# Performance work log

Measured on AMD Instinct MI355X. Metric: run time of the kernel, lower is better.

## Reference

```python
import jax, jax.numpy as jnp
import numpy as np

B, S, D, H = 2, 2048, 1024, 16
DK = D // H  # 64

def setup_inputs() -> dict:
    key = jax.random.key(0)
    ks = jax.random.split(key, 12)
    scale = 1.0 / np.sqrt(D)
    return {
        "q": jax.random.normal(ks[0], (B, S, D), jnp.float32),
        "k": jax.random.normal(ks[1], (B, S, D), jnp.float32),
        "v": jax.random.normal(ks[2], (B, S, D), jnp.float32),
        "Wq": jax.random.normal(ks[3], (D, D), jnp.float32) * scale,
        "bq": jnp.zeros((D,), jnp.float32),
        "Wk": jax.random.normal(ks[4], (D, D), jnp.float32) * scale,
        "bk": jnp.zeros((D,), jnp.float32),
        "Wv": jax.random.normal(ks[5], (D, D), jnp.float32) * scale,
        "bv": jnp.zeros((D,), jnp.float32),
        "Wo": jax.random.normal(ks[6], (D, D), jnp.float32) * scale,
        "bo": jnp.zeros((D,), jnp.float32),
        "mask": jnp.ones((B, 1, S, S), jnp.bool_),
    }

def reference(q, k, v, Wq, bq, Wk, bk, Wv, bv, Wo, bo, mask):
    # Linear projections: y = x @ W^T + b (torch nn.Linear convention)
    def proj(x, W, b):
        return x @ W.T + b
    # [B,S,D] -> [B,H,S,DK]
    def split_heads(x):
        return x.reshape(B, S, H, DK).transpose(0, 2, 1, 3)

    query = split_heads(proj(q, Wq, bq))
    key_ = split_heads(proj(k, Wk, bk))
    value = split_heads(proj(v, Wv, bv))

    # NOTE: original uses out-of-place masked_fill whose result is discarded,
    # so mask has no effect on the computation (reproduced faithfully here).
    scores = jnp.einsum('bhqd,bhkd->bhqk', query, key_) / jnp.sqrt(
        jnp.asarray(DK, query.dtype))
    attn = jax.nn.softmax(scores, axis=-1)  # dropout p=0.0: identity
    x = jnp.einsum('bhqk,bhkd->bhqd', attn, value)
    x = x.transpose(0, 2, 1, 3).reshape(B, S, D)
    return proj(x, Wo, bo)
```

## Files before the change

### kernel.cpp

```cpp
#include <hip/hip_runtime.h>
#include <hip/hip_bf16.h>


typedef __attribute__((ext_vector_type(8))) short bf16x8;
typedef __attribute__((ext_vector_type(4))) float f32x4;
typedef unsigned short u16;
typedef unsigned int u32;

#define MFMA16(a, b, c) __builtin_amdgcn_mfma_f32_16x16x32_bf16(a, b, c, 0, 0, 0)
#define EXP2(x) __builtin_amdgcn_exp2f(x)

static __device__ __forceinline__ u16 f2bf(float f) {
    union { __hip_bfloat16 h; u16 u; } v;
    v.h = __float2bfloat16(f);
    return v.u;
}

static __device__ __forceinline__ u16 f2bf_fast(float f) {
    return (u16)((__float_as_uint(f) + 0x8000u) >> 16);
}

static __device__ __forceinline__ void gload16(const u16* g, u16* l) {
    __builtin_amdgcn_global_load_lds(
        (const __attribute__((address_space(1))) void*)g,
        (__attribute__((address_space(3))) void*)l, 16, 0, 0);
}

struct CvtArgs { const float* in[4]; u16* out[4]; };

__global__ __launch_bounds__(256)
void cvt_multi(CvtArgs a, int bp)
{
    const int tsel = blockIdx.x / bp;
    const int i = ((blockIdx.x % bp) * 256 + threadIdx.x) * 8;
    const float* in = a.in[tsel];
    u16* out = a.out[tsel];
    float4 x = *(const float4*)(in + i);
    float4 y = *(const float4*)(in + i + 4);
    u16 o[8];
    o[0]=f2bf(x.x); o[1]=f2bf(x.y); o[2]=f2bf(x.z); o[3]=f2bf(x.w);
    o[4]=f2bf(y.x); o[5]=f2bf(y.y); o[6]=f2bf(y.z); o[7]=f2bf(y.w);
    *(uint4*)(out + i) = *(uint4*)o;
}

struct GemmArgs {
    const u16* A[3]; const u16* W[3]; const float* bias[3];
    u16* C[3]; float osc[3]; int epi[3];
};

__global__ __launch_bounds__(256)
void gemm_qkv(GemmArgs g)
{
    __shared__ u16 lds_a[2][128 * 32];
    __shared__ u16 lds_b[2][128 * 32];

    const int z = blockIdx.y;
    const u16* Ap = g.A[z];
    const u16* Wp = g.W[z];
    const int epi = g.epi[z];

    const int t    = threadIdx.x;
    const int lane = t & 63;
    const int w    = t >> 6;
    const int wm   = w >> 1, wn = w & 1;
    const int ll   = lane & 15;
    const int lg   = lane >> 4;

    const int tile_m = (epi == 1 ? (blockIdx.x & 7) : (blockIdx.x >> 3)) * 128;
    const int tile_n = (epi == 1 ? (blockIdx.x >> 3) : (blockIdx.x & 7)) * 128;

    const int c0   = w * 2;
    const int lrow = lane >> 2;
    const int lcol = (lane & 3) * 8;

    f32x4 acc[4][4] = {};

    #define STAGE(buf, kt)                                                     \
    {                                                                          \
        _Pragma("unroll")                                                      \
        for (int j = 0; j < 2; j++) {                                          \
            const int c = c0 + j;                                              \
            gload16(Ap + (size_t)(tile_m + c * 16 + lrow) * 1024 + (kt) + lcol,\
                    &lds_a[buf][c * 512]);                                     \
            gload16(Wp + (size_t)(tile_n + c * 16 + lrow) * 1024 + (kt) + lcol,\
                    &lds_b[buf][c * 512]);                                     \
        }                                                                      \
    }

    STAGE(0, 0);
    __syncthreads();

    int cur = 0;
    for (int kt = 0; kt < 1024; kt += 32) {
        if (kt + 32 < 1024) STAGE(cur ^ 1, kt + 32);

        bf16x8 af[4], bfr[4];
        #pragma unroll
        for (int i = 0; i < 4; i++)
            af[i] = *(bf16x8*)&lds_a[cur][(wm * 64 + i * 16 + ll) * 32 + lg * 8];
        #pragma unroll
        for (int j = 0; j < 4; j++)
            bfr[j] = *(bf16x8*)&lds_b[cur][(wn * 64 + j * 16 + ll) * 32 + lg * 8];
        #pragma unroll
        for (int i = 0; i < 4; i++)
            #pragma unroll
            for (int j = 0; j < 4; j++)
                acc[i][j] = MFMA16(af[i], bfr[j], acc[i][j]);

        __syncthreads();
        cur ^= 1;
    }
    #undef STAGE

    const float osc = g.osc[z];
    const float* bias = g.bias[z];
    u16* Cp = g.C[z];

    #pragma unroll
    for (int i = 0; i < 4; i++) {
        const int row0 = tile_m + wm * 64 + i * 16 + lg * 4;
        #pragma unroll
        for (int j = 0; j < 4; j++) {
            const int col = tile_n + wn * 64 + j * 16 + ll;
            if (epi == 1) {
                const int b = col >> 11, s = col & 2047;
                #pragma unroll
                for (int r = 0; r < 4; r++)
                    Cp[(size_t)(b * 1024 + row0 + r) * 2048 + s] =
                        f2bf(acc[i][j][r] + bias[row0 + r]);
            } else {
                const float bias_v = bias[col];
                const int h = col >> 6, dk = col & 63;
                const int b = row0 >> 11;
                #pragma unroll
                for (int r = 0; r < 4; r++) {
                    const int s = (row0 + r) & 2047;
                    Cp[((size_t)(b * 16 + h) * 2048 + s) * 64 + dk] =
                        f2bf((acc[i][j][r] + bias_v) * osc);
                }
            }
        }
    }
}

__global__ __launch_bounds__(256)
void gemm_out(const u16* __restrict__ Ap, const u16* __restrict__ Wp,
              const float* __restrict__ bias, float* __restrict__ Cp)
{
    __shared__ u16 lds_a[2][128 * 32];
    __shared__ u16 lds_b[2][64 * 32];

    const int t    = threadIdx.x;
    const int lane = t & 63;
    const int w    = t >> 6;
    const int wm   = w >> 1, wn = w & 1;
    const int ll   = lane & 15;
    const int lg   = lane >> 4;

    const int tile_m = (blockIdx.x >> 4) * 128;
    const int tile_n = (blockIdx.x & 15) * 64;

    const int lrow = lane >> 2;
    const int lcol = (lane & 3) * 8;

    f32x4 acc[4][2] = {};

    #define OSTAGE(buf, kt)                                                    \
    {                                                                          \
        _Pragma("unroll")                                                      \
        for (int j = 0; j < 3; j++) {                                          \
            const int c = w * 3 + j;                                           \
            if (c < 8) {                                                       \
                const int row = tile_m + c * 16 + lrow;                        \
                const int col = (kt) + lcol;                                   \
                const u16* ga = Ap + ((size_t)((row >> 11) * 16 + (col >> 6))  \
                                      * 2048 + (row & 2047)) * 64 + (col & 63);\
                gload16(ga, &lds_a[buf][c * 512]);                             \
            } else {                                                           \
                const int cc = c - 8;                                          \
                gload16(Wp + (size_t)(tile_n + cc * 16 + lrow) * 1024          \
                        + (kt) + lcol, &lds_b[buf][cc * 512]);                 \
            }                                                                  \
        }                                                                      \
    }

    OSTAGE(0, 0);
    __syncthreads();

    int cur = 0;
    for (int kt = 0; kt < 1024; kt += 32) {
        if (kt + 32 < 1024) OSTAGE(cur ^ 1, kt + 32);

        bf16x8 af[4], bfr[2];
        #pragma unroll
        for (int i = 0; i < 4; i++)
            af[i] = *(bf16x8*)&lds_a[cur][(wm * 64 + i * 16 + ll) * 32 + lg * 8];
        #pragma unroll
        for (int j = 0; j < 2; j++)
            bfr[j] = *(bf16x8*)&lds_b[cur][(wn * 32 + j * 16 + ll) * 32 + lg * 8];
        #pragma unroll
        for (int i = 0; i < 4; i++)
            #pragma unroll
            for (int j = 0; j < 2; j++)
                acc[i][j] = MFMA16(af[i], bfr[j], acc[i][j]);

        __syncthreads();
        cur ^= 1;
    }
    #undef OSTAGE

    #pragma unroll
    for (int i = 0; i < 4; i++) {
        const int row0 = tile_m + wm * 64 + i * 16 + lg * 4;
        #pragma unroll
        for (int j = 0; j < 2; j++) {
            const int col = tile_n + wn * 32 + j * 16 + ll;
            const float bias_v = bias[col];
            #pragma unroll
            for (int r = 0; r < 4; r++)
                Cp[(size_t)(row0 + r) * 1024 + col] = acc[i][j][r] + bias_v;
        }
    }
}

__global__ __launch_bounds__(512)
void attn_kernel(const u16* __restrict__ Qh, const u16* __restrict__ Kh,
                 const u16* __restrict__ Vt, u16* __restrict__ Oh)
{
    __shared__ u16 lds_k[2][64 * 64];
    __shared__ u16 lds_v[2][64 * 64];
    __shared__ u16 lds_p[8][16 * 64];

    const int t    = threadIdx.x;
    const int lane = t & 63;
    const int w    = t >> 6;
    const int ll   = lane & 15;
    const int lg   = lane >> 4;
    const int r7   = ll & 7;

    const int qt = blockIdx.x & 15;
    const int bh = blockIdx.x >> 4;
    const int q0 = qt * 128 + w * 16;

    const u16* Qbase = Qh + ((size_t)bh * 2048 + q0 + ll) * 64 + lg * 8;
    const bf16x8 bq0 = *(const bf16x8*)(Qbase);
    const bf16x8 bq1 = *(const bf16x8*)(Qbase + 32);

    bf16x8 bones;
    #pragma unroll
    for (int i = 0; i < 8; i++) bones[i] = (short)0x3F80;

    f32x4 acc[4] = {};
    f32x4 acc_l = {};
    float m_run = 0.f;

    const int srow = lane >> 3;
    const int scol = 8 * ((lane & 7) ^ srow);
    const u16* Kg = Kh + (size_t)bh * 2048 * 64;
    const u16* Vg = Vt + (size_t)bh * 64 * 2048;

    #define ASTAGE(buf, kt)                                                    \
    {                                                                          \
        const int rr = w * 8 + srow;                                           \
        gload16(Kg + (size_t)((kt) + rr) * 64 + scol, &lds_k[buf][w * 512]);   \
        gload16(Vg + (size_t)rr * 2048 + (kt) + scol, &lds_v[buf][w * 512]);   \
    }

    ASTAGE(0, 0);
    __syncthreads();

    u16* lp = lds_p[w];
    int cur = 0;

    for (int kt = 0; kt < 2048; kt += 64) {
        if (kt + 64 < 2048) ASTAGE(cur ^ 1, kt + 64);

        f32x4 s[4];
        #pragma unroll
        for (int ks = 0; ks < 4; ks++) {
            const u16* kp = &lds_k[cur][(ks * 16 + ll) * 64];
            const bf16x8 ak0 = *(const bf16x8*)(kp + ((lg * 8)      ^ (r7 * 8)));
            const bf16x8 ak1 = *(const bf16x8*)(kp + ((lg * 8 + 32) ^ (r7 * 8)));
            f32x4 z = {-m_run, -m_run, -m_run, -m_run};
            z = MFMA16(ak0, bq0, z);
            z = MFMA16(ak1, bq1, z);
            s[ks] = z;
        }

        float m0 = fmaxf(fmaxf(s[0][0], s[0][1]), s[0][2]);
        float m1 = fmaxf(fmaxf(s[0][3], s[1][0]), s[1][1]);
        float m2 = fmaxf(fmaxf(s[1][2], s[1][3]), s[2][0]);
        float m3 = fmaxf(fmaxf(s[2][1], s[2][2]), s[2][3]);
        float m4 = fmaxf(fmaxf(s[3][0], s[3][1]), s[3][2]);
        float mx = fmaxf(fmaxf(fmaxf(m0, m1), fmaxf(m2, m3)),
                         fmaxf(m4, s[3][3]));
        mx = fmaxf(mx, __shfl_xor(mx, 16));
        mx = fmaxf(mx, __shfl_xor(mx, 32));

        if (!__all(mx <= 11.0f)) {
            const float dsh = fmaxf(mx, 0.f);
            const float es = EXP2(-dsh);
            m_run += dsh;
            #pragma unroll
            for (int r = 0; r < 4; r++) {
                const float esq = __shfl(es, lg * 4 + r);
                #pragma unroll
                for (int dt = 0; dt < 4; dt++) acc[dt][r] *= esq;
                acc_l[r] *= esq;
            }
            #pragma unroll
            for (int ks = 0; ks < 4; ks++) {
                u16 pk[4];
                #pragma unroll
                for (int r = 0; r < 4; r++) pk[r] = f2bf_fast(EXP2(s[ks][r] - dsh));
                *(uint2*)&lp[ll * 64 + ((ks * 16 + lg * 4) ^ (r7 * 8))] = *(uint2*)pk;
            }
        } else {
            #pragma unroll
            for (int ks = 0; ks < 4; ks++) {
                u16 pk[4];
                #pragma unroll
                for (int r = 0; r < 4; r++) pk[r] = f2bf_fast(EXP2(s[ks][r]));
                *(uint2*)&lp[ll * 64 + ((ks * 16 + lg * 4) ^ (r7 * 8))] = *(uint2*)pk;
            }
        }

        #pragma unroll
        for (int ks2 = 0; ks2 < 2; ks2++) {
            const int so = (ks2 * 32 + lg * 8) ^ (r7 * 8);
            const bf16x8 pa = *(const bf16x8*)&lp[ll * 64 + so];
            #pragma unroll
            for (int dt = 0; dt < 4; dt++) {
                const bf16x8 bv = *(const bf16x8*)&lds_v[cur][(dt * 16 + ll) * 64 + so];
                acc[dt] = MFMA16(pa, bv, acc[dt]);
            }
            acc_l = MFMA16(pa, bones, acc_l);
        }

        __syncthreads();
        cur ^= 1;
    }
    #undef ASTAGE

    #pragma unroll
    for (int r = 0; r < 4; r++) {
        const float lq = 1.f / acc_l[r];
        const int qg = q0 + lg * 4 + r;
        u16* Op = Oh + ((size_t)bh * 2048 + qg) * 64 + ll;
        #pragma unroll
        for (int dt = 0; dt < 4; dt++)
            Op[dt * 16] = f2bf(acc[dt][r] * lq);
    }
}

extern "C" void kernel_launch(void* const* d_in, const int* in_sizes, int n_in,
                              void* d_out, int out_size, void* d_ws, size_t ws_size,
                              hipStream_t stream) {
    const float* q  = (const float*)d_in[0];
    const float* k  = (const float*)d_in[1];
    const float* v  = (const float*)d_in[2];
    const float* Wq = (const float*)d_in[3];
    const float* bq = (const float*)d_in[4];
    const float* Wk = (const float*)d_in[5];
    const float* bk = (const float*)d_in[6];
    const float* Wv = (const float*)d_in[7];
    const float* bv = (const float*)d_in[8];
    const float* Wo = (const float*)d_in[9];
    const float* bo = (const float*)d_in[10];
    float* out = (float*)d_out;

    const size_t M4 = (size_t)4 * 1024 * 1024;
    const size_t M1 = (size_t)1024 * 1024;
    const float qscale = 0.18033688011112042f;
    const dim3 blk(256);

    if (ws_size >= (size_t)56 * 1024 * 1024) {
        u16* Xq  = (u16*)d_ws;
        u16* Xk  = Xq + M4;
        u16* Xv  = Xk + M4;
        u16* Qh  = Xv + M4;
        u16* Kh  = Qh + M4;
        u16* Vtb = Kh + M4;
        u16* Wqb = Vtb + M4;
        u16* Wkb = Wqb + M1;
        u16* Wvb = Wkb + M1;
        u16* Wob = Wvb + M1;
        u16* Oh  = Xq;

        CvtArgs cw; cw.in[0]=Wq; cw.in[1]=Wk; cw.in[2]=Wv; cw.in[3]=Wo;
        cw.out[0]=Wqb; cw.out[1]=Wkb; cw.out[2]=Wvb; cw.out[3]=Wob;
        cvt_multi<<<4 * 512, blk, 0, stream>>>(cw, 512);

        CvtArgs cx; cx.in[0]=q; cx.in[1]=k; cx.in[2]=v; cx.in[3]=q;
        cx.out[0]=Xq; cx.out[1]=Xk; cx.out[2]=Xv; cx.out[3]=Xq;
        cvt_multi<<<3 * 2048, blk, 0, stream>>>(cx, 2048);

        GemmArgs ga;
        ga.A[0]=Xq;  ga.A[1]=Xk;  ga.A[2]=Wvb;
        ga.W[0]=Wqb; ga.W[1]=Wkb; ga.W[2]=Xv;
        ga.bias[0]=bq; ga.bias[1]=bk; ga.bias[2]=bv;
        ga.C[0]=Qh; ga.C[1]=Kh; ga.C[2]=Vtb;
        ga.osc[0]=qscale; ga.osc[1]=1.0f; ga.osc[2]=1.0f;
        ga.epi[0]=3; ga.epi[1]=3; ga.epi[2]=1;
        gemm_qkv<<<dim3(256, 3), blk, 0, stream>>>(ga);

        attn_kernel<<<512, dim3(512), 0, stream>>>(Qh, Kh, Vtb, Oh);

        gemm_out<<<512, blk, 0, stream>>>(Oh, Wob, bo, out);
    } else {
        u16* X   = (u16*)d_ws;
        u16* Qh  = X + M4;
        u16* Kh  = Qh + M4;
        u16* Vtb = Kh + M4;
        u16* Wqb = Vtb + M4;
        u16* Wkb = Wqb + M1;
        u16* Wvb = Wkb + M1;
        u16* Wob = Wvb + M1;

        CvtArgs cw; cw.in[0]=Wq; cw.in[1]=Wk; cw.in[2]=Wv; cw.in[3]=Wo;
        cw.out[0]=Wqb; cw.out[1]=Wkb; cw.out[2]=Wvb; cw.out[3]=Wob;
        cvt_multi<<<4 * 512, blk, 0, stream>>>(cw, 512);

        const float* srcs[3] = {q, k, v};
        for (int i = 0; i < 3; i++) {
            CvtArgs cx; cx.in[0]=srcs[i]; cx.out[0]=X;
            cx.in[1]=cx.in[2]=cx.in[3]=srcs[i]; cx.out[1]=cx.out[2]=cx.out[3]=X;
            cvt_multi<<<2048, blk, 0, stream>>>(cx, 2048);
            GemmArgs ga;
            for (int z = 0; z < 3; z++) {
                if (i == 2) { ga.A[z]=Wvb; ga.W[z]=X;  ga.C[z]=Vtb; ga.bias[z]=bv; ga.osc[z]=1.0f; ga.epi[z]=1; }
                else if (i == 0) { ga.A[z]=X; ga.W[z]=Wqb; ga.C[z]=Qh; ga.bias[z]=bq; ga.osc[z]=qscale; ga.epi[z]=3; }
                else { ga.A[z]=X; ga.W[z]=Wkb; ga.C[z]=Kh; ga.bias[z]=bk; ga.osc[z]=1.0f; ga.epi[z]=3; }
            }
            gemm_qkv<<<dim3(256, 1), blk, 0, stream>>>(ga);
        }

        attn_kernel<<<512, dim3(512), 0, stream>>>(Qh, Kh, Vtb, X);

        gemm_out<<<512, blk, 0, stream>>>(X, Wob, bo, out);
    }
}
```

Before: 145.5 us.

## Merge conversions into one launch, swizzle block IDs, and prioritize MFMA phases

Merges the weight and activation fp32-to-bf16 conversions into a single launch of 16 equal-size slices, saving one kernel launch. Remaps block indices in both GEMMs and the attention kernel with an XCD-aware swizzle, so that consecutive blocks sharing the same data land on the same chiplet's L2. In attention it raises wave priority around the MFMA sections with s_setprio. It also skips the cross-lane max reduction unless the rescale branch is actually taken. The per-lane __all check stays equivalent because the row max is only needed when rescaling.

```diff
diff --git a/kernel.cpp b/kernel.cpp
--- a/kernel.cpp
+++ b/kernel.cpp
@@ -26,13 +26,13 @@
         (__attribute__((address_space(3))) void*)l, 16, 0, 0);
 }
 
-struct CvtArgs { const float* in[4]; u16* out[4]; };
+struct CvtArgs16 { const float* in[16]; u16* out[16]; };
 
 __global__ __launch_bounds__(256)
-void cvt_multi(CvtArgs a, int bp)
+void cvt_multi(CvtArgs16 a)
 {
-    const int tsel = blockIdx.x / bp;
-    const int i = ((blockIdx.x % bp) * 256 + threadIdx.x) * 8;
+    const int tsel = blockIdx.x >> 9;
+    const int i = (((blockIdx.x & 511) * 256) + threadIdx.x) * 8;
     const float* in = a.in[tsel];
     u16* out = a.out[tsel];
     float4 x = *(const float4*)(in + i);
@@ -66,8 +66,10 @@
     const int ll   = lane & 15;
     const int lg   = lane >> 4;
 
-    const int tile_m = (epi == 1 ? (blockIdx.x & 7) : (blockIdx.x >> 3)) * 128;
-    const int tile_n = (epi == 1 ? (blockIdx.x >> 3) : (blockIdx.x & 7)) * 128;
+    const int bx  = blockIdx.x;
+    const int swz = (bx & 7) * 32 + (bx >> 3);
+    const int tile_m = (epi == 1 ? (swz & 7) : (swz >> 3)) * 128;
+    const int tile_n = (epi == 1 ? (swz >> 3) : (swz & 7)) * 128;
 
     const int c0   = w * 2;
     const int lrow = lane >> 2;
@@ -157,8 +159,10 @@
     const int ll   = lane & 15;
     const int lg   = lane >> 4;
 
-    const int tile_m = (blockIdx.x >> 4) * 128;
-    const int tile_n = (blockIdx.x & 15) * 64;
+    const int bx  = blockIdx.x;
+    const int swz = (bx & 7) * 64 + (bx >> 3);
+    const int tile_m = (swz >> 4) * 128;
+    const int tile_n = (swz & 15) * 64;
 
     const int lrow = lane >> 2;
     const int lcol = (lane & 3) * 8;
@@ -238,8 +242,10 @@
     const int lg   = lane >> 4;
     const int r7   = ll & 7;
 
-    const int qt = blockIdx.x & 15;
-    const int bh = blockIdx.x >> 4;
+    const int bx  = blockIdx.x;
+    const int swz = (bx & 7) * 64 + (bx >> 3);
+    const int qt = swz & 15;
+    const int bh = swz >> 4;
     const int q0 = qt * 128 + w * 16;
 
     const u16* Qbase = Qh + ((size_t)bh * 2048 + q0 + ll) * 64 + lg * 8;
@@ -276,6 +282,7 @@
         if (kt + 64 < 2048) ASTAGE(cur ^ 1, kt + 64);
 
         f32x4 s[4];
+        __builtin_amdgcn_s_setprio(1);
         #pragma unroll
         for (int ks = 0; ks < 4; ks++) {
             const u16* kp = &lds_k[cur][(ks * 16 + ll) * 64];
@@ -286,6 +293,7 @@
             z = MFMA16(ak1, bq1, z);
             s[ks] = z;
         }
+        __builtin_amdgcn_s_setprio(0);
 
         float m0 = fmaxf(fmaxf(s[0][0], s[0][1]), s[0][2]);
         float m1 = fmaxf(fmaxf(s[0][3], s[1][0]), s[1][1]);
@@ -294,11 +302,11 @@
         float m4 = fmaxf(fmaxf(s[3][0], s[3][1]), s[3][2]);
         float mx = fmaxf(fmaxf(fmaxf(m0, m1), fmaxf(m2, m3)),
                          fmaxf(m4, s[3][3]));
-        mx = fmaxf(mx, __shfl_xor(mx, 16));
-        mx = fmaxf(mx, __shfl_xor(mx, 32));
 
         if (!__all(mx <= 11.0f)) {
-            const float dsh = fmaxf(mx, 0.f);
+            float rmx = fmaxf(mx, __shfl_xor(mx, 16));
+            rmx = fmaxf(rmx, __shfl_xor(rmx, 32));
+            const float dsh = fmaxf(rmx, 0.f);
             const float es = EXP2(-dsh);
             m_run += dsh;
             #pragma unroll
@@ -325,6 +333,7 @@
             }
         }
 
+        __builtin_amdgcn_s_setprio(1);
         #pragma unroll
         for (int ks2 = 0; ks2 < 2; ks2++) {
             const int so = (ks2 * 32 + lg * 8) ^ (r7 * 8);
@@ -336,6 +345,7 @@
             }
             acc_l = MFMA16(pa, bones, acc_l);
         }
+        __builtin_amdgcn_s_setprio(0);
 
         __syncthreads();
         cur ^= 1;
@@ -387,13 +397,17 @@
         u16* Wob = Wvb + M1;
         u16* Oh  = Xq;
 
-        CvtArgs cw; cw.in[0]=Wq; cw.in[1]=Wk; cw.in[2]=Wv; cw.in[3]=Wo;
-        cw.out[0]=Wqb; cw.out[1]=Wkb; cw.out[2]=Wvb; cw.out[3]=Wob;
-        cvt_multi<<<4 * 512, blk, 0, stream>>>(cw, 512);
-
-        CvtArgs cx; cx.in[0]=q; cx.in[1]=k; cx.in[2]=v; cx.in[3]=q;
-        cx.out[0]=Xq; cx.out[1]=Xk; cx.out[2]=Xv; cx.out[3]=Xq;
-        cvt_multi<<<3 * 2048, blk, 0, stream>>>(cx, 2048);
+        CvtArgs16 cv;
+        cv.in[0]=Wq; cv.out[0]=Wqb;
+        cv.in[1]=Wk; cv.out[1]=Wkb;
+        cv.in[2]=Wv; cv.out[2]=Wvb;
+        cv.in[3]=Wo; cv.out[3]=Wob;
+        for (int j = 0; j < 4; j++) {
+            cv.in[4 + j]  = q + (size_t)j * M1;  cv.out[4 + j]  = Xq + (size_t)j * M1;
+            cv.in[8 + j]  = k + (size_t)j * M1;  cv.out[8 + j]  = Xk + (size_t)j * M1;
+            cv.in[12 + j] = v + (size_t)j * M1;  cv.out[12 + j] = Xv + (size_t)j * M1;
+        }
+        cvt_multi<<<16 * 512, blk, 0, stream>>>(cv);
 
         GemmArgs ga;
         ga.A[0]=Xq;  ga.A[1]=Xk;  ga.A[2]=Wvb;
@@ -417,15 +431,21 @@
         u16* Wvb = Wkb + M1;
         u16* Wob = Wvb + M1;
 
-        CvtArgs cw; cw.in[0]=Wq; cw.in[1]=Wk; cw.in[2]=Wv; cw.in[3]=Wo;
-        cw.out[0]=Wqb; cw.out[1]=Wkb; cw.out[2]=Wvb; cw.out[3]=Wob;
-        cvt_multi<<<4 * 512, blk, 0, stream>>>(cw, 512);
+        CvtArgs16 cw;
+        for (int j = 0; j < 16; j++) { cw.in[j] = Wq; cw.out[j] = Wqb; }
+        cw.in[0]=Wq; cw.out[0]=Wqb; cw.in[1]=Wk; cw.out[1]=Wkb;
+        cw.in[2]=Wv; cw.out[2]=Wvb; cw.in[3]=Wo; cw.out[3]=Wob;
+        cvt_multi<<<4 * 512, blk, 0, stream>>>(cw);
 
         const float* srcs[3] = {q, k, v};
         for (int i = 0; i < 3; i++) {
-            CvtArgs cx; cx.in[0]=srcs[i]; cx.out[0]=X;
-            cx.in[1]=cx.in[2]=cx.in[3]=srcs[i]; cx.out[1]=cx.out[2]=cx.out[3]=X;
-            cvt_multi<<<2048, blk, 0, stream>>>(cx, 2048);
+            CvtArgs16 cx;
+            for (int j = 0; j < 16; j++) { cx.in[j] = srcs[i]; cx.out[j] = X; }
+            for (int j = 0; j < 4; j++) {
+                cx.in[j]  = srcs[i] + (size_t)j * M1;
+                cx.out[j] = X + (size_t)j * M1;
+            }
+            cvt_multi<<<4 * 512, blk, 0, stream>>>(cx);
             GemmArgs ga;
             for (int z = 0; z < 3; z++) {
                 if (i == 2) { ga.A[z]=Wvb; ga.W[z]=X;  ga.C[z]=Vtb; ga.bias[z]=bv; ga.osc[z]=1.0f; ga.epi[z]=1; }
```

New measurement: 130.2 us. -10.5%, faster.
